# Performance work log

Hardware: AMD Instinct MI355X
Metric: run time of the kernel (lower is better)

## Reference

```python
import jax, jax.numpy as jnp
import numpy as np

ALPHA = 0.2
NEG_BIG = -9e15


def setup_inputs() -> dict:
    key = jax.random.key(0)
    k1, k2, k3, k4 = jax.random.split(key, 4)
    N, F_in, F_out = 8192, 512, 128
    h = jax.random.normal(k1, (N, F_in), dtype=jnp.float32)
    adj = jax.random.randint(k2, (N, N), 0, 2, dtype=jnp.int32)
    W = jax.random.normal(k3, (F_in, F_out), dtype=jnp.float32) * 0.05
    a = jax.random.normal(k4, (2 * F_out, 1), dtype=jnp.float32) * 0.05
    return {"h": h, "adj": adj, "W": W, "a": a}


def reference(h, adj, W, a):
    F_out = W.shape[1]
    Wh = h @ W                                  # [N, F_out]
    Wh1 = Wh @ a[:F_out, :]                     # [N, 1]
    Wh2 = Wh @ a[F_out:, :]                     # [N, 1]
    e = Wh1 + Wh2.T                             # [N, N] broadcast add
    e = jnp.where(e >= 0, e, ALPHA * e)         # LeakyReLU
    scores = jnp.where(adj > 0, e, NEG_BIG)     # adjacency mask
    attention = jax.nn.softmax(scores, axis=1)  # row-wise softmax
    h_prime = attention @ Wh                    # [N, F_out]
    return jax.nn.elu(h_prime)                  # concat=True -> elu
```

## Files before the change

### kernel.cpp

```cpp
#include <hip/hip_runtime.h>
#include <stdint.h>

typedef float f32x4 __attribute__((ext_vector_type(4)));
typedef __bf16 bf16x8 __attribute__((ext_vector_type(8)));
typedef unsigned short u16;
typedef unsigned int u32;

#define N_NODES 8192
#define F_IN 512
#define F_OUT 128
#define LRA 0.2f

__device__ __forceinline__ u16 f32_to_bf16(float f) {
  union { float f; u32 u; } v; v.f = f;
  u32 u = v.u;
  u += 0x7fffu + ((u >> 16) & 1u);
  return (u16)(u >> 16);
}
__device__ __forceinline__ float bf16_to_f32(u16 h) {
  union { u32 u; float f; } v; v.u = ((u32)h) << 16;
  return v.f;
}
__device__ __forceinline__ float dot4(f32x4 a, f32x4 b) {
  return a[0] * b[0] + a[1] * b[1] + a[2] * b[2] + a[3] * b[3];
}

__global__ __launch_bounds__(256) void prep_k(
    const float* __restrict__ W, const float* __restrict__ av,
    u16* __restrict__ WT, float* __restrict__ wa) {
  __shared__ u16 Ts[F_OUT][40];
  const int t = threadIdx.x, kc = (int)blockIdx.x * 32;
  {
    const int k = t >> 3, dof = (t & 7) * 16;
#pragma unroll
    for (int q = 0; q < 4; ++q) {
      f32x4 v = *(const f32x4*)&W[(size_t)(kc + k) * F_OUT + dof + q * 4];
#pragma unroll
      for (int e = 0; e < 4; ++e) Ts[dof + q * 4 + e][k] = f32_to_bf16(v[e]);
    }
  }
  __syncthreads();
  {
    const int d = t >> 1, kh = (t & 1) * 16;
    uint4 o0 = *(uint4*)&Ts[d][kh];
    uint4 o1 = *(uint4*)&Ts[d][kh + 8];
    *(uint4*)&WT[(size_t)d * F_IN + kc + kh] = o0;
    *(uint4*)&WT[(size_t)d * F_IN + kc + kh + 8] = o1;
  }
  {
    const int kl = t >> 3, l8 = t & 7;
    const float* wrow = &W[(size_t)(kc + kl) * F_OUT];
    float s1 = 0.f, s2 = 0.f;
#pragma unroll
    for (int q = 0; q < 2; ++q) {
      int dd = l8 * 16 + q * 8;
      f32x4 w0 = *(const f32x4*)&wrow[dd];
      f32x4 w1 = *(const f32x4*)&wrow[dd + 4];
      s1 += dot4(w0, *(const f32x4*)&av[dd]) + dot4(w1, *(const f32x4*)&av[dd + 4]);
      s2 += dot4(w0, *(const f32x4*)&av[F_OUT + dd]) + dot4(w1, *(const f32x4*)&av[F_OUT + dd + 4]);
    }
#pragma unroll
    for (int m = 1; m <= 4; m <<= 1) {
      s1 += __shfl_xor(s1, m, 64);
      s2 += __shfl_xor(s2, m, 64);
    }
    if (l8 == 0) { wa[kc + kl] = s1; wa[F_IN + kc + kl] = s2; }
  }
}

__global__ __launch_bounds__(256) void gemm_wh(
    const float* __restrict__ h, const u16* __restrict__ WT,
    const float* __restrict__ wa,
    u16* __restrict__ WhT, float* __restrict__ Wh1, float* __restrict__ Wh2) {
  __shared__ u16 Ab[2][32][80];
  __shared__ u16 Bs[2][F_OUT][80];
  const int t = threadIdx.x;
  const int i0 = (int)blockIdx.x * 32;
  const int w = t >> 6, l = t & 63, r = l & 15, oct = l >> 4;
  const int mrow = (w & 1) * 16, ncol = (w >> 1) * 64;
  const int ar = t >> 3, ak = (t & 7) * 8;
  const int br = t >> 1, bk = (t & 1) * 32;

  const float* hrow = &h[(size_t)(i0 + ar) * F_IN + ak];
  const u16* wtrow = &WT[(size_t)br * F_IN + bk];
  const float* wap = &wa[ak];
  const float* wbp = &wa[F_IN + ak];

  f32x4 acc[4];
#pragma unroll
  for (int nf = 0; nf < 4; ++nf) acc[nf] = (f32x4){0.f, 0.f, 0.f, 0.f};
  float s1 = 0.f, s2 = 0.f;

  f32x4 ra0, ra1;
  uint4 rb[4];

#define STORE_A(B)                                                        \
  { u32 p0 = f32_to_bf16(ra0[0]) | ((u32)f32_to_bf16(ra0[1]) << 16);      \
    u32 p1 = f32_to_bf16(ra0[2]) | ((u32)f32_to_bf16(ra0[3]) << 16);      \
    u32 p2 = f32_to_bf16(ra1[0]) | ((u32)f32_to_bf16(ra1[1]) << 16);      \
    u32 p3 = f32_to_bf16(ra1[2]) | ((u32)f32_to_bf16(ra1[3]) << 16);      \
    uint4 v; v.x = p0; v.y = p1; v.z = p2; v.w = p3;                      \
    *(uint4*)&Ab[B][ar][ak] = v; }
#define STORE_B(B)                                                        \
  { *(uint4*)&Bs[B][br][bk + 0]  = rb[0];                                 \
    *(uint4*)&Bs[B][br][bk + 8]  = rb[1];                                 \
    *(uint4*)&Bs[B][br][bk + 16] = rb[2];                                 \
    *(uint4*)&Bs[B][br][bk + 24] = rb[3]; }

  ra0 = *(const f32x4*)&hrow[0];
  ra1 = *(const f32x4*)&hrow[4];
#pragma unroll
  for (int j = 0; j < 4; ++j) rb[j] = *(const uint4*)&wtrow[j * 8];
  s1 += dot4(ra0, *(const f32x4*)&wap[0]) + dot4(ra1, *(const f32x4*)&wap[4]);
  s2 += dot4(ra0, *(const f32x4*)&wbp[0]) + dot4(ra1, *(const f32x4*)&wbp[4]);
  STORE_A(0); STORE_B(0);
  __syncthreads();

#pragma unroll
  for (int it = 0; it < 8; ++it) {
    const int buf = it & 1;
    if (it < 7) {
      const int kc = (it + 1) * 64;
      ra0 = *(const f32x4*)&hrow[kc];
      ra1 = *(const f32x4*)&hrow[kc + 4];
#pragma unroll
      for (int j = 0; j < 4; ++j) rb[j] = *(const uint4*)&wtrow[kc + j * 8];
      s1 += dot4(ra0, *(const f32x4*)&wap[kc]) + dot4(ra1, *(const f32x4*)&wap[kc + 4]);
      s2 += dot4(ra0, *(const f32x4*)&wbp[kc]) + dot4(ra1, *(const f32x4*)&wbp[kc + 4]);
    }
#pragma unroll
    for (int ks = 0; ks < 2; ++ks) {
      bf16x8 af = *(bf16x8*)&Ab[buf][mrow + r][ks * 32 + oct * 8];
#pragma unroll
      for (int nf = 0; nf < 4; ++nf) {
        bf16x8 bfv = *(bf16x8*)&Bs[buf][ncol + nf * 16 + r][ks * 32 + oct * 8];
        acc[nf] = __builtin_amdgcn_mfma_f32_16x16x32_bf16(af, bfv, acc[nf], 0, 0, 0);
      }
    }
    if (it < 7) {
      STORE_A(buf ^ 1); STORE_B(buf ^ 1);
      __syncthreads();
    }
  }
#undef STORE_A
#undef STORE_B

#pragma unroll
  for (int m = 1; m <= 4; m <<= 1) {
    s1 += __shfl_xor(s1, m, 64);
    s2 += __shfl_xor(s2, m, 64);
  }
  if ((t & 7) == 0) { Wh1[i0 + ar] = s1; Wh2[i0 + ar] = s2; }

#pragma unroll
  for (int nf = 0; nf < 4; ++nf) {
    u32 lo = f32_to_bf16(acc[nf][0]) | ((u32)f32_to_bf16(acc[nf][1]) << 16);
    u32 hi = f32_to_bf16(acc[nf][2]) | ((u32)f32_to_bf16(acc[nf][3]) << 16);
    const int d = ncol + nf * 16 + r;
    uint2 v; v.x = lo; v.y = hi;
    *(uint2*)&WhT[(size_t)d * N_NODES + i0 + mrow + oct * 4] = v;
  }
}

__global__ __launch_bounds__(256) void gat_main(
    const int* __restrict__ adj, const float* __restrict__ Wh1,
    const float* __restrict__ Wh2, const u16* __restrict__ WhT,
    float* __restrict__ accp, float* __restrict__ sp,
    const int js, const int jlen) {
  __shared__ u16 Plds[2][64][80];
  __shared__ float sscr[256];

  const int t = threadIdx.x;
  const int bi = (int)blockIdx.x / js;
  const int jsi = (int)blockIdx.x % js;
  const int i0 = bi * 64;
  const int j0 = jsi * jlen;

  const int il = t >> 2, q4 = (t & 3) * 16;
  const float cI = Wh1[i0 + il];
  const int w = t >> 6, l = t & 63, r = l & 15, oct = l >> 4;

  const u16* vp0 = &WhT[(size_t)(w * 32 + r) * N_NODES];
  const u16* vp1 = &WhT[(size_t)(w * 32 + 16 + r) * N_NODES];

  f32x4 acc[4][2];
#pragma unroll
  for (int it = 0; it < 4; ++it)
#pragma unroll
    for (int dt = 0; dt < 2; ++dt) acc[it][dt] = (f32x4){0.f, 0.f, 0.f, 0.f};
  float sAcc = 0.f;

  for (int ch = 0; ch < jlen; ch += 64) {
    const int jc = j0 + ch;
    const int buf = (ch >> 6) & 1;

    bf16x8 b00 = *(const bf16x8*)&vp0[jc + oct * 8];
    bf16x8 b01 = *(const bf16x8*)&vp0[jc + 32 + oct * 8];
    bf16x8 b10 = *(const bf16x8*)&vp1[jc + oct * 8];
    bf16x8 b11 = *(const bf16x8*)&vp1[jc + 32 + oct * 8];

    const int* arow = &adj[(size_t)(i0 + il) * N_NODES + jc + q4];
    const float* w2p = &Wh2[jc + q4];
#pragma unroll
    for (int k = 0; k < 4; ++k) {
      int4 a4 = *(const int4*)&arow[k * 4];
      f32x4 w2 = *(const f32x4*)&w2p[k * 4];
      int ai[4] = {a4.x, a4.y, a4.z, a4.w};
      u16 pu[4];
#pragma unroll
      for (int e = 0; e < 4; ++e) {
        float x = cI + w2[e];
        x = x >= 0.f ? x : LRA * x;
        float p = __expf(x);
        p = ai[e] ? p : 0.f;
        u16 b = f32_to_bf16(p);
        pu[e] = b;
        sAcc += bf16_to_f32(b);
      }
      ushort4 pv; pv.x = pu[0]; pv.y = pu[1]; pv.z = pu[2]; pv.w = pu[3];
      *(ushort4*)&Plds[buf][il][q4 + k * 4] = pv;
    }
    __syncthreads();

#pragma unroll
    for (int ks = 0; ks < 2; ++ks) {
      bf16x8 bA = ks ? b01 : b00;
      bf16x8 bB = ks ? b11 : b10;
#pragma unroll
      for (int it = 0; it < 4; ++it) {
        bf16x8 af = *(bf16x8*)&Plds[buf][it * 16 + r][ks * 32 + oct * 8];
        acc[it][0] = __builtin_amdgcn_mfma_f32_16x16x32_bf16(af, bA, acc[it][0], 0, 0, 0);
        acc[it][1] = __builtin_amdgcn_mfma_f32_16x16x32_bf16(af, bB, acc[it][1], 0, 0, 0);
      }
    }
  }

  sscr[t] = sAcc;
  __syncthreads();
  if (t < 64) {
    float s = sscr[4 * t] + sscr[4 * t + 1] + sscr[4 * t + 2] + sscr[4 * t + 3];
    sp[(size_t)jsi * N_NODES + i0 + t] = s;
  }

#pragma unroll
  for (int it = 0; it < 4; ++it) {
#pragma unroll
    for (int dt = 0; dt < 2; ++dt) {
#pragma unroll
      for (int rr = 0; rr < 4; ++rr) {
        int row = i0 + it * 16 + oct * 4 + rr;
        int dcol = w * 32 + dt * 16 + r;
        accp[((size_t)jsi * N_NODES + row) * F_OUT + dcol] = acc[it][dt][rr];
      }
    }
  }
}

__global__ __launch_bounds__(256) void finalize_k(
    const float* __restrict__ accp, const float* __restrict__ sp,
    float* __restrict__ out, const int js) {
  const int idx = (int)blockIdx.x * 256 + threadIdx.x;
  const int i = idx >> 7;
  float num = 0.f, den = 0.f;
  for (int s = 0; s < js; ++s) {
    num += accp[(size_t)s * (N_NODES * F_OUT) + idx];
    den += sp[(size_t)s * N_NODES + i];
  }
  float x = num / den;
  out[idx] = x > 0.f ? x : expm1f(x);
}

extern "C" void kernel_launch(void* const* d_in, const int* in_sizes, int n_in,
                              void* d_out, int out_size, void* d_ws, size_t ws_size,
                              hipStream_t stream) {
  const float* h = (const float*)d_in[0];
  const int* adj = (const int*)d_in[1];
  const float* W = (const float*)d_in[2];
  const float* av = (const float*)d_in[3];
  float* out = (float*)d_out;
  char* ws = (char*)d_ws;

  u16* WT = (u16*)ws;
  float* wa = (float*)(ws + (256ull << 10));
  u16* WhT = (u16*)(ws + (512ull << 10));
  float* Wh1 = (float*)(ws + (512ull << 10) + (2ull << 20));
  float* Wh2 = (float*)(ws + (512ull << 10) + (2ull << 20) + (32ull << 10));
  float* sp = (float*)(ws + (512ull << 10) + (2ull << 20) + (64ull << 10));
  float* accp = (float*)(ws + (512ull << 10) + (2ull << 20) + (320ull << 10));
  const size_t base = (512ull << 10) + (2ull << 20) + (320ull << 10);

  int js = 8;
  while (js > 1 && base + (size_t)js * N_NODES * F_OUT * 4 > ws_size) js >>= 1;
  const int jlen = N_NODES / js;

  prep_k<<<16, 256, 0, stream>>>(W, av, WT, wa);
  gemm_wh<<<N_NODES / 32, 256, 0, stream>>>(h, WT, wa, WhT, Wh1, Wh2);
  gat_main<<<(N_NODES / 64) * js, 256, 0, stream>>>(adj, Wh1, Wh2, WhT, accp, sp, js, jlen);
  finalize_k<<<(N_NODES * F_OUT) / 256, 256, 0, stream>>>(accp, sp, out, js);
}
```

Before: 113.3 us.

## Compute attention fragments in registers per wave, drop LDS staging and barriers

Restructures gat_main so each wave owns 16 rows and builds its bf16 P fragment directly in MFMA operand layout in registers. This removes the shared-memory P buffer and the per-chunk __syncthreads. Wh2 is staged once into LDS, adjacency loads are software-prefetched one chunk ahead with nontemporal hints, and each wave now loads all 128 WhT columns itself. The bf16 row-sum becomes an fp32 sum, which slightly changes the softmax normalization, and finalize_k is vectorized to float4. In exchange, WhT traffic per block rises fourfold and the 32KB LDS allocation plus the occupancy hint may limit residency.

New measurement: 195.7 us. 72.7% more time.

```diff
diff --git a/kernel.cpp b/kernel.cpp
--- a/kernel.cpp
+++ b/kernel.cpp
@@ -3,6 +3,7 @@
 
 typedef float f32x4 __attribute__((ext_vector_type(4)));
 typedef __bf16 bf16x8 __attribute__((ext_vector_type(8)));
+typedef int i32x4 __attribute__((ext_vector_type(4)));
 typedef unsigned short u16;
 typedef unsigned int u32;
 
@@ -16,10 +17,6 @@
   u32 u = v.u;
   u += 0x7fffu + ((u >> 16) & 1u);
   return (u16)(u >> 16);
-}
-__device__ __forceinline__ float bf16_to_f32(u16 h) {
-  union { u32 u; float f; } v; v.u = ((u32)h) << 16;
-  return v.f;
 }
 __device__ __forceinline__ float dot4(f32x4 a, f32x4 b) {
   return a[0] * b[0] + a[1] * b[1] + a[2] * b[2] + a[3] * b[3];
@@ -162,112 +159,113 @@
   }
 }
 
-__global__ __launch_bounds__(256) void gat_main(
+__global__ __launch_bounds__(256, 3) void gat_main(
     const int* __restrict__ adj, const float* __restrict__ Wh1,
     const float* __restrict__ Wh2, const u16* __restrict__ WhT,
     float* __restrict__ accp, float* __restrict__ sp,
     const int js, const int jlen) {
-  __shared__ u16 Plds[2][64][80];
-  __shared__ float sscr[256];
-
+  __shared__ float w2s[8192];
   const int t = threadIdx.x;
   const int bi = (int)blockIdx.x / js;
   const int jsi = (int)blockIdx.x % js;
-  const int i0 = bi * 64;
   const int j0 = jsi * jlen;
-
-  const int il = t >> 2, q4 = (t & 3) * 16;
-  const float cI = Wh1[i0 + il];
-  const int w = t >> 6, l = t & 63, r = l & 15, oct = l >> 4;
-
-  const u16* vp0 = &WhT[(size_t)(w * 32 + r) * N_NODES];
-  const u16* vp1 = &WhT[(size_t)(w * 32 + 16 + r) * N_NODES];
-
-  f32x4 acc[4][2];
-#pragma unroll
-  for (int it = 0; it < 4; ++it)
-#pragma unroll
-    for (int dt = 0; dt < 2; ++dt) acc[it][dt] = (f32x4){0.f, 0.f, 0.f, 0.f};
+  const int w = t >> 6, l = t & 63;
+  const int r = l & 15, oct = l >> 4;
+  const int i0w = bi * 64 + w * 16;
+
+  for (int k = t * 4; k < jlen; k += 1024)
+    *(f32x4*)&w2s[k] = *(const f32x4*)&Wh2[j0 + k];
+  const float cI = Wh1[i0w + r];
+  __syncthreads();
+
+  const i32x4* arow = (const i32x4*)&adj[(size_t)(i0w + r) * N_NODES + j0 + oct * 8];
+  const u16* vbase = &WhT[(size_t)r * N_NODES + j0 + oct * 8];
+
+  f32x4 acc[8];
+#pragma unroll
+  for (int d = 0; d < 8; ++d) acc[d] = (f32x4){0.f, 0.f, 0.f, 0.f};
   float sAcc = 0.f;
 
+  i32x4 pa[4];
+#pragma unroll
+  for (int q = 0; q < 4; ++q)
+    pa[q] = __builtin_nontemporal_load(&arow[(q >> 1) * 8 + (q & 1)]);
+
   for (int ch = 0; ch < jlen; ch += 64) {
-    const int jc = j0 + ch;
-    const int buf = (ch >> 6) & 1;
-
-    bf16x8 b00 = *(const bf16x8*)&vp0[jc + oct * 8];
-    bf16x8 b01 = *(const bf16x8*)&vp0[jc + 32 + oct * 8];
-    bf16x8 b10 = *(const bf16x8*)&vp1[jc + oct * 8];
-    bf16x8 b11 = *(const bf16x8*)&vp1[jc + 32 + oct * 8];
-
-    const int* arow = &adj[(size_t)(i0 + il) * N_NODES + jc + q4];
-    const float* w2p = &Wh2[jc + q4];
-#pragma unroll
-    for (int k = 0; k < 4; ++k) {
-      int4 a4 = *(const int4*)&arow[k * 4];
-      f32x4 w2 = *(const f32x4*)&w2p[k * 4];
-      int ai[4] = {a4.x, a4.y, a4.z, a4.w};
-      u16 pu[4];
-#pragma unroll
-      for (int e = 0; e < 4; ++e) {
-        float x = cI + w2[e];
-        x = x >= 0.f ? x : LRA * x;
-        float p = __expf(x);
-        p = ai[e] ? p : 0.f;
-        u16 b = f32_to_bf16(p);
-        pu[e] = b;
-        sAcc += bf16_to_f32(b);
+    i32x4 ca[4];
+#pragma unroll
+    for (int q = 0; q < 4; ++q) ca[q] = pa[q];
+    if (ch + 64 < jlen) {
+      const i32x4* an = arow + ((ch + 64) >> 2);
+#pragma unroll
+      for (int q = 0; q < 4; ++q)
+        pa[q] = __builtin_nontemporal_load(&an[(q >> 1) * 8 + (q & 1)]);
+    }
+
+#pragma unroll
+    for (int ks = 0; ks < 2; ++ks) {
+      const u16* vp = vbase + ch + ks * 32;
+      bf16x8 bv[8];
+#pragma unroll
+      for (int df = 0; df < 8; ++df)
+        bv[df] = *(const bf16x8*)(vp + (size_t)df * 16 * N_NODES);
+
+      f32x4 w20 = *(const f32x4*)&w2s[ch + ks * 32 + oct * 8];
+      f32x4 w21 = *(const f32x4*)&w2s[ch + ks * 32 + oct * 8 + 4];
+      union { u32 u[4]; bf16x8 v; } afu;
+      float ps = 0.f;
+#pragma unroll
+      for (int e2 = 0; e2 < 4; ++e2) {
+        float wa2 = (e2 < 2) ? w20[2 * e2] : w21[2 * e2 - 4];
+        float wb2 = (e2 < 2) ? w20[2 * e2 + 1] : w21[2 * e2 - 3];
+        int a0 = ca[ks * 2 + (e2 >> 1)][(e2 & 1) * 2];
+        int a1 = ca[ks * 2 + (e2 >> 1)][(e2 & 1) * 2 + 1];
+        float x0 = cI + wa2; x0 = fmaxf(x0, LRA * x0);
+        float x1 = cI + wb2; x1 = fmaxf(x1, LRA * x1);
+        float p0 = a0 ? __expf(x0) : 0.f;
+        float p1 = a1 ? __expf(x1) : 0.f;
+        ps += p0 + p1;
+        afu.u[e2] = (u32)f32_to_bf16(p0) | ((u32)f32_to_bf16(p1) << 16);
       }
-      ushort4 pv; pv.x = pu[0]; pv.y = pu[1]; pv.z = pu[2]; pv.w = pu[3];
-      *(ushort4*)&Plds[buf][il][q4 + k * 4] = pv;
-    }
-    __syncthreads();
-
-#pragma unroll
-    for (int ks = 0; ks < 2; ++ks) {
-      bf16x8 bA = ks ? b01 : b00;
-      bf16x8 bB = ks ? b11 : b10;
-#pragma unroll
-      for (int it = 0; it < 4; ++it) {
-        bf16x8 af = *(bf16x8*)&Plds[buf][it * 16 + r][ks * 32 + oct * 8];
-        acc[it][0] = __builtin_amdgcn_mfma_f32_16x16x32_bf16(af, bA, acc[it][0], 0, 0, 0);
-        acc[it][1] = __builtin_amdgcn_mfma_f32_16x16x32_bf16(af, bB, acc[it][1], 0, 0, 0);
-      }
-    }
-  }
-
-  sscr[t] = sAcc;
-  __syncthreads();
-  if (t < 64) {
-    float s = sscr[4 * t] + sscr[4 * t + 1] + sscr[4 * t + 2] + sscr[4 * t + 3];
-    sp[(size_t)jsi * N_NODES + i0 + t] = s;
-  }
-
-#pragma unroll
-  for (int it = 0; it < 4; ++it) {
-#pragma unroll
-    for (int dt = 0; dt < 2; ++dt) {
-#pragma unroll
-      for (int rr = 0; rr < 4; ++rr) {
-        int row = i0 + it * 16 + oct * 4 + rr;
-        int dcol = w * 32 + dt * 16 + r;
-        accp[((size_t)jsi * N_NODES + row) * F_OUT + dcol] = acc[it][dt][rr];
-      }
-    }
-  }
+      sAcc += ps;
+
+#pragma unroll
+      for (int df = 0; df < 8; ++df)
+        acc[df] = __builtin_amdgcn_mfma_f32_16x16x32_bf16(afu.v, bv[df], acc[df], 0, 0, 0);
+    }
+  }
+
+  float s = sAcc;
+  s += __shfl_xor(s, 16, 64);
+  s += __shfl_xor(s, 32, 64);
+  if (l < 16) sp[(size_t)jsi * N_NODES + i0w + l] = s;
+
+  float* ap = &accp[((size_t)jsi * N_NODES + i0w + oct * 4) * F_OUT + r];
+#pragma unroll
+  for (int df = 0; df < 8; ++df)
+#pragma unroll
+    for (int rr = 0; rr < 4; ++rr)
+      __builtin_nontemporal_store(acc[df][rr], ap + (size_t)rr * F_OUT + df * 16);
 }
 
 __global__ __launch_bounds__(256) void finalize_k(
     const float* __restrict__ accp, const float* __restrict__ sp,
     float* __restrict__ out, const int js) {
-  const int idx = (int)blockIdx.x * 256 + threadIdx.x;
-  const int i = idx >> 7;
-  float num = 0.f, den = 0.f;
+  const int vidx = (int)blockIdx.x * 256 + threadIdx.x;
+  const int i = vidx >> 5;
+  f32x4 num = (f32x4){0.f, 0.f, 0.f, 0.f};
+  float den = 0.f;
   for (int s = 0; s < js; ++s) {
-    num += accp[(size_t)s * (N_NODES * F_OUT) + idx];
+    num += __builtin_nontemporal_load((const f32x4*)accp + (size_t)s * (N_NODES * F_OUT / 4) + vidx);
     den += sp[(size_t)s * N_NODES + i];
   }
-  float x = num / den;
-  out[idx] = x > 0.f ? x : expm1f(x);
+  f32x4 o;
+#pragma unroll
+  for (int c = 0; c < 4; ++c) {
+    float x = num[c] / den;
+    o[c] = x > 0.f ? x : expm1f(x);
+  }
+  *((f32x4*)out + vidx) = o;
 }
 
 extern "C" void kernel_launch(void* const* d_in, const int* in_sizes, int n_in,
@@ -296,5 +294,5 @@
   prep_k<<<16, 256, 0, stream>>>(W, av, WT, wa);
   gemm_wh<<<N_NODES / 32, 256, 0, stream>>>(h, WT, wa, WhT, Wh1, Wh2);
   gat_main<<<(N_NODES / 64) * js, 256, 0, stream>>>(adj, Wh1, Wh2, WhT, accp, sp, js, jlen);
-  finalize_k<<<(N_NODES * F_OUT) / 256, 256, 0, stream>>>(accp, sp, out, js);
-}
+  finalize_k<<<(N_NODES * F_OUT) / 1024, 256, 0, stream>>>(accp, sp, out, js);
+}
```

## Prefetch adjacency tiles in registers, widen chunks, swizzle LDS, vectorize finalize

Applied to the files above, without the earlier changes.

Reworks the attention kernel so each wave owns 16 rows and prefetches the next chunk's adjacency values into registers while computing the current one. The chunk grows from 64 to 128 columns, and the Wh1 and Wh2 slices are cached in shared memory. The P tile uses an XOR-swizzled shared-memory layout instead of padding, and the row-sum denominators are reduced with wave shuffles. The finalize kernel is vectorized to four floats per thread. The split count is fixed at compile time, which drops the workspace-size fallback, and the register prefetch raises register pressure.

Measured after the change: 204.8 us. +80.7%, slower.

```diff
diff --git a/kernel.cpp b/kernel.cpp
--- a/kernel.cpp
+++ b/kernel.cpp
@@ -3,6 +3,7 @@
 
 typedef float f32x4 __attribute__((ext_vector_type(4)));
 typedef __bf16 bf16x8 __attribute__((ext_vector_type(8)));
+typedef int i32x2 __attribute__((ext_vector_type(2)));
 typedef unsigned short u16;
 typedef unsigned int u32;
 
@@ -10,16 +11,15 @@
 #define F_IN 512
 #define F_OUT 128
 #define LRA 0.2f
+#define JS 8
+#define JLEN (N_NODES / JS)
+#define CHUNK 128
 
 __device__ __forceinline__ u16 f32_to_bf16(float f) {
   union { float f; u32 u; } v; v.f = f;
   u32 u = v.u;
   u += 0x7fffu + ((u >> 16) & 1u);
   return (u16)(u >> 16);
-}
-__device__ __forceinline__ float bf16_to_f32(u16 h) {
-  union { u32 u; float f; } v; v.u = ((u32)h) << 16;
-  return v.f;
 }
 __device__ __forceinline__ float dot4(f32x4 a, f32x4 b) {
   return a[0] * b[0] + a[1] * b[1] + a[2] * b[2] + a[3] * b[3];
@@ -162,84 +162,100 @@
   }
 }
 
+__device__ __forceinline__ void stage_tile(
+    char* plds, const int* abase, const float* w2s, const float* w1s,
+    i32x2 (&areg)[16], float (&sden)[16],
+    int w, int l, int ch, int chn, bool pref) {
+#pragma unroll
+  for (int rr = 0; rr < 16; ++rr) {
+    i32x2 a2 = areg[rr];
+    if (pref)
+      areg[rr] = *(const i32x2*)(abase + (size_t)rr * N_NODES + chn + l * 2);
+    const int row = w * 16 + rr;
+    float cR = w1s[row];
+    float xa = cR + w2s[ch + l * 2];
+    float xb = cR + w2s[ch + l * 2 + 1];
+    xa = fmaxf(xa, LRA * xa);
+    xb = fmaxf(xb, LRA * xb);
+    float pa = a2[0] ? __expf(xa) : 0.f;
+    float pb = a2[1] ? __expf(xb) : 0.f;
+    u32 ua = f32_to_bf16(pa), ub = f32_to_bf16(pb);
+    union { u32 u; float f; } fa, fb;
+    fa.u = ua << 16; fb.u = ub << 16;
+    sden[rr] += fa.f + fb.f;
+    u32 pk = ua | (ub << 16);
+    u32 bo = (u32)(row * (CHUNK * 2) + l * 4) ^ ((u32)(row & 7) << 4);
+    *(u32*)(plds + bo) = pk;
+  }
+}
+
 __global__ __launch_bounds__(256) void gat_main(
     const int* __restrict__ adj, const float* __restrict__ Wh1,
     const float* __restrict__ Wh2, const u16* __restrict__ WhT,
-    float* __restrict__ accp, float* __restrict__ sp,
-    const int js, const int jlen) {
-  __shared__ u16 Plds[2][64][80];
-  __shared__ float sscr[256];
+    float* __restrict__ accp, float* __restrict__ sp) {
+  __shared__ u16 Plds[2][64][CHUNK];
+  __shared__ float w2s[JLEN];
+  __shared__ float w1s[64];
 
   const int t = threadIdx.x;
-  const int bi = (int)blockIdx.x / js;
-  const int jsi = (int)blockIdx.x % js;
+  const int bi = (int)blockIdx.x / JS;
+  const int jsi = (int)blockIdx.x % JS;
   const int i0 = bi * 64;
-  const int j0 = jsi * jlen;
-
-  const int il = t >> 2, q4 = (t & 3) * 16;
-  const float cI = Wh1[i0 + il];
+  const int j0 = jsi * JLEN;
   const int w = t >> 6, l = t & 63, r = l & 15, oct = l >> 4;
 
-  const u16* vp0 = &WhT[(size_t)(w * 32 + r) * N_NODES];
-  const u16* vp1 = &WhT[(size_t)(w * 32 + 16 + r) * N_NODES];
+  for (int k = t * 4; k < JLEN; k += 1024)
+    *(f32x4*)&w2s[k] = *(const f32x4*)&Wh2[j0 + k];
+  if (t < 64) w1s[t] = Wh1[i0 + t];
+  __syncthreads();
+
+  const int* abase = &adj[(size_t)(i0 + w * 16) * N_NODES + j0];
+  const u16* vb0 = &WhT[(size_t)(w * 32 + r) * N_NODES + j0 + oct * 8];
+  const u16* vb1 = &WhT[(size_t)(w * 32 + 16 + r) * N_NODES + j0 + oct * 8];
 
   f32x4 acc[4][2];
 #pragma unroll
   for (int it = 0; it < 4; ++it)
 #pragma unroll
     for (int dt = 0; dt < 2; ++dt) acc[it][dt] = (f32x4){0.f, 0.f, 0.f, 0.f};
-  float sAcc = 0.f;
-
-  for (int ch = 0; ch < jlen; ch += 64) {
-    const int jc = j0 + ch;
-    const int buf = (ch >> 6) & 1;
-
-    bf16x8 b00 = *(const bf16x8*)&vp0[jc + oct * 8];
-    bf16x8 b01 = *(const bf16x8*)&vp0[jc + 32 + oct * 8];
-    bf16x8 b10 = *(const bf16x8*)&vp1[jc + oct * 8];
-    bf16x8 b11 = *(const bf16x8*)&vp1[jc + 32 + oct * 8];
-
-    const int* arow = &adj[(size_t)(i0 + il) * N_NODES + jc + q4];
-    const float* w2p = &Wh2[jc + q4];
-#pragma unroll
-    for (int k = 0; k < 4; ++k) {
-      int4 a4 = *(const int4*)&arow[k * 4];
-      f32x4 w2 = *(const f32x4*)&w2p[k * 4];
-      int ai[4] = {a4.x, a4.y, a4.z, a4.w};
-      u16 pu[4];
-#pragma unroll
-      for (int e = 0; e < 4; ++e) {
-        float x = cI + w2[e];
-        x = x >= 0.f ? x : LRA * x;
-        float p = __expf(x);
-        p = ai[e] ? p : 0.f;
-        u16 b = f32_to_bf16(p);
-        pu[e] = b;
-        sAcc += bf16_to_f32(b);
+  float sden[16];
+#pragma unroll
+  for (int rr = 0; rr < 16; ++rr) sden[rr] = 0.f;
+
+  i32x2 areg[16];
+#pragma unroll
+  for (int rr = 0; rr < 16; ++rr)
+    areg[rr] = *(const i32x2*)(abase + (size_t)rr * N_NODES + l * 2);
+
+  int buf = 0;
+  for (int ch = 0; ch < JLEN; ch += CHUNK) {
+    const bool more = (ch + CHUNK) < JLEN;
+    stage_tile((char*)&Plds[buf][0][0], abase, w2s, w1s, areg, sden,
+               w, l, ch, ch + CHUNK, more);
+    __syncthreads();
+
+#pragma unroll
+    for (int ks = 0; ks < 4; ++ks) {
+      bf16x8 b0 = *(const bf16x8*)(vb0 + ch + ks * 32);
+      bf16x8 b1 = *(const bf16x8*)(vb1 + ch + ks * 32);
+      const u32 go = (u32)(((u32)(ks * 4 + oct) ^ (u32)(r & 7)) << 4);
+#pragma unroll
+      for (int it = 0; it < 4; ++it) {
+        u32 ro = (u32)((it * 16 + r) * (CHUNK * 2)) + go;
+        bf16x8 af = *(bf16x8*)((char*)&Plds[buf][0][0] + ro);
+        acc[it][0] = __builtin_amdgcn_mfma_f32_16x16x32_bf16(af, b0, acc[it][0], 0, 0, 0);
+        acc[it][1] = __builtin_amdgcn_mfma_f32_16x16x32_bf16(af, b1, acc[it][1], 0, 0, 0);
       }
-      ushort4 pv; pv.x = pu[0]; pv.y = pu[1]; pv.z = pu[2]; pv.w = pu[3];
-      *(ushort4*)&Plds[buf][il][q4 + k * 4] = pv;
-    }
-    __syncthreads();
-
-#pragma unroll
-    for (int ks = 0; ks < 2; ++ks) {
-      bf16x8 bA = ks ? b01 : b00;
-      bf16x8 bB = ks ? b11 : b10;
-#pragma unroll
-      for (int it = 0; it < 4; ++it) {
-        bf16x8 af = *(bf16x8*)&Plds[buf][it * 16 + r][ks * 32 + oct * 8];
-        acc[it][0] = __builtin_amdgcn_mfma_f32_16x16x32_bf16(af, bA, acc[it][0], 0, 0, 0);
-        acc[it][1] = __builtin_amdgcn_mfma_f32_16x16x32_bf16(af, bB, acc[it][1], 0, 0, 0);
-      }
-    }
-  }
-
-  sscr[t] = sAcc;
-  __syncthreads();
-  if (t < 64) {
-    float s = sscr[4 * t] + sscr[4 * t + 1] + sscr[4 * t + 2] + sscr[4 * t + 3];
-    sp[(size_t)jsi * N_NODES + i0 + t] = s;
+    }
+    buf ^= 1;
+  }
+
+#pragma unroll
+  for (int rr = 0; rr < 16; ++rr) {
+    float s = sden[rr];
+#pragma unroll
+    for (int m = 1; m <= 32; m <<= 1) s += __shfl_xor(s, m, 64);
+    if (l == rr) sp[(size_t)jsi * N_NODES + i0 + w * 16 + rr] = s;
   }
 
 #pragma unroll
@@ -258,16 +274,23 @@
 
 __global__ __launch_bounds__(256) void finalize_k(
     const float* __restrict__ accp, const float* __restrict__ sp,
-    float* __restrict__ out, const int js) {
-  const int idx = (int)blockIdx.x * 256 + threadIdx.x;
-  const int i = idx >> 7;
-  float num = 0.f, den = 0.f;
-  for (int s = 0; s < js; ++s) {
-    num += accp[(size_t)s * (N_NODES * F_OUT) + idx];
+    float* __restrict__ out) {
+  const int vidx = (int)blockIdx.x * 256 + threadIdx.x;
+  const int i = vidx >> 5;
+  f32x4 num = (f32x4){0.f, 0.f, 0.f, 0.f};
+  float den = 0.f;
+#pragma unroll
+  for (int s = 0; s < JS; ++s) {
+    num += *((const f32x4*)accp + (size_t)s * (N_NODES * F_OUT / 4) + vidx);
     den += sp[(size_t)s * N_NODES + i];
   }
-  float x = num / den;
-  out[idx] = x > 0.f ? x : expm1f(x);
+  f32x4 o;
+#pragma unroll
+  for (int c = 0; c < 4; ++c) {
+    float x = num[c] / den;
+    o[c] = x > 0.f ? x : expm1f(x);
+  }
+  *((f32x4*)out + vidx) = o;
 }
 
 extern "C" void kernel_launch(void* const* d_in, const int* in_sizes, int n_in,
@@ -287,14 +310,9 @@
   float* Wh2 = (float*)(ws + (512ull << 10) + (2ull << 20) + (32ull << 10));
   float* sp = (float*)(ws + (512ull << 10) + (2ull << 20) + (64ull << 10));
   float* accp = (float*)(ws + (512ull << 10) + (2ull << 20) + (320ull << 10));
-  const size_t base = (512ull << 10) + (2ull << 20) + (320ull << 10);
-
-  int js = 8;
-  while (js > 1 && base + (size_t)js * N_NODES * F_OUT * 4 > ws_size) js >>= 1;
-  const int jlen = N_NODES / js;
 
   prep_k<<<16, 256, 0, stream>>>(W, av, WT, wa);
   gemm_wh<<<N_NODES / 32, 256, 0, stream>>>(h, WT, wa, WhT, Wh1, Wh2);
-  gat_main<<<(N_NODES / 64) * js, 256, 0, stream>>>(adj, Wh1, Wh2, WhT, accp, sp, js, jlen);
-  finalize_k<<<(N_NODES * F_OUT) / 256, 256, 0, stream>>>(accp, sp, out, js);
-}
+  gat_main<<<(N_NODES / 64) * JS, 256, 0, stream>>>(adj, Wh1, Wh2, WhT, accp, sp);
+  finalize_k<<<(N_NODES * F_OUT) / 1024, 256, 0, stream>>>(accp, sp, out);
+}
```
